# Optimization experiments

Measured on AMD Instinct MI355X. Metric: run time of the kernel, lower is better.

The kernel has to match this reference:

```python
import jax, jax.numpy as jnp
from jax import lax
import numpy as np


def setup_inputs() -> dict:
    key = jax.random.key(0)
    k1, k2, k3, k4 = jax.random.split(key, 4)
    X = jax.random.normal(k1, (2_000_000, 20), dtype=jnp.float32)
    W = jax.random.normal(k2, (20, 20), dtype=jnp.float32) * 0.1  # Linear weight
    b = jax.random.normal(k3, (20,), dtype=jnp.float32) * 0.1     # Linear bias
    rand_weight = jax.random.uniform(k4, (20, 20), dtype=jnp.float32)  # fixed, non-trainable
    return {"X": X, "W": W, "b": b, "rand_weight": rand_weight}


def reference(X, W, b, rand_weight):
    # X = self.liner(X)  -> torch Linear: X @ W.T + b
    h = X @ W.T + b
    # X = relu(X @ rand_weight + 1)
    h = jax.nn.relu(h @ rand_weight + 1.0)
    # (second self.liner(X) in the source is computed but unused -> omitted)
    # while X.abs().sum() > 1: X /= 2  -- count halvings, then apply once.
    s0 = jnp.sum(jnp.abs(h))
    def cond(c):
        _, s = c
        return s > 1.0
    def body(c):
        n, s = c
        return n + 1, s * 0.5
    n, _ = lax.while_loop(cond, body, (jnp.int32(0), s0))
    h = h * jnp.exp2(-n.astype(h.dtype))  # exact power-of-two scaling == repeated /2
    return jnp.sum(h)
```

## Files before the change

### kernel.cpp

```cpp
#include <hip/hip_runtime.h>


#define D 20
#define BLOCK 256
#define RPT 2
#define RPB (BLOCK * RPT)
#define F4PB (RPB * D / 4)
#define NLD (F4PB / BLOCK)
#define LDS_F4 (F4PB + F4PB / 10)
#define WS_PARTIALS_BYTES 32768


__global__ void setup_kernel(const float* __restrict__ W,
                             const float* __restrict__ b,
                             const float* __restrict__ RW,
                             float* __restrict__ Mt,
                             float* __restrict__ dvec,
                             unsigned* __restrict__ counter) {
    const int tid = threadIdx.x;
    if (tid == 0) *counter = 0u;
    for (int idx = tid; idx < D * D; idx += blockDim.x) {
        const int j = idx / D, k = idx % D;
        float s = 0.0f;
        for (int i = 0; i < D; ++i)
            s = fmaf(W[i * D + k], RW[i * D + j], s);
        Mt[idx] = s;
    }
    if (tid < D) {
        float s = 1.0f;
        for (int i = 0; i < D; ++i)
            s = fmaf(b[i], RW[i * D + tid], s);
        dvec[tid] = s;
    }
}

__global__ void __launch_bounds__(BLOCK)
fused_mlp_sum(const float* __restrict__ X,
              const float* __restrict__ Mt,
              const float* __restrict__ dvec,
              double* __restrict__ partials,
              unsigned* __restrict__ counter,
              float* __restrict__ out,
              int nrows) {
    __shared__ float4 lds4[LDS_F4];
    __shared__ float wave_sums[BLOCK / 64];
    __shared__ double dsum[BLOCK / 64];
    __shared__ int is_last;

    const int tid = threadIdx.x;
    const int bid = blockIdx.x;

    const long long total_f4 = ((long long)nrows * D) >> 2;
    const long long base_f4 = (long long)bid * F4PB;
    const long long rem = total_f4 - base_f4;
    const int chunk_f4 = (rem < (long long)F4PB) ? (int)rem : F4PB;
    const float4* __restrict__ xg = (const float4*)X + base_f4;

#pragma unroll
    for (int q = 0; q < NLD; ++q) {
        const int s = tid + BLOCK * q;
        const int sc = (s < chunk_f4) ? s : (chunk_f4 - 1);
        lds4[s + s / 10] = xg[sc];
    }
    __syncthreads();

    float x0[D], x1[D];
    const int b4 = 11 * tid;
#pragma unroll
    for (int q = 0; q < 5; ++q) {
        const float4 v = lds4[b4 + q];
        x0[4 * q + 0] = v.x; x0[4 * q + 1] = v.y;
        x0[4 * q + 2] = v.z; x0[4 * q + 3] = v.w;
        const float4 u = lds4[b4 + 5 + q];
        x1[4 * q + 0] = u.x; x1[4 * q + 1] = u.y;
        x1[4 * q + 2] = u.z; x1[4 * q + 3] = u.w;
    }

    float lsum = 0.0f;
#pragma unroll
    for (int j = 0; j < D; ++j) {
        float t0 = dvec[j];
        float t1 = t0;
#pragma unroll
        for (int k = 0; k < D; ++k) {
            const float m = Mt[j * D + k];
            t0 = fmaf(x0[k], m, t0);
            t1 = fmaf(x1[k], m, t1);
        }
        lsum += fmaxf(t0, 0.0f) + fmaxf(t1, 0.0f);
    }
    const bool valid = (long long)bid * RPB + 2 * tid < (long long)nrows;
    lsum = valid ? lsum : 0.0f;

#pragma unroll
    for (int off = 32; off > 0; off >>= 1)
        lsum += __shfl_down(lsum, off, 64);
    if ((tid & 63) == 0) wave_sums[tid >> 6] = lsum;
    __syncthreads();

    if (tid == 0) {
        float bs = wave_sums[0] + wave_sums[1] + wave_sums[2] + wave_sums[3];
        __hip_atomic_store(&partials[bid], (double)bs, __ATOMIC_RELEASE,
                           __HIP_MEMORY_SCOPE_AGENT);
        const unsigned t = __hip_atomic_fetch_add(counter, 1u, __ATOMIC_ACQ_REL,
                                                  __HIP_MEMORY_SCOPE_AGENT);
        is_last = (t == gridDim.x - 1);
    }
    __syncthreads();

    if (is_last) {
        double s = 0.0;
        for (int i = tid; i < (int)gridDim.x; i += BLOCK)
            s += __hip_atomic_load(&partials[i], __ATOMIC_RELAXED,
                                   __HIP_MEMORY_SCOPE_AGENT);
#pragma unroll
        for (int off = 32; off > 0; off >>= 1)
            s += __shfl_down(s, off, 64);
        if ((tid & 63) == 0) dsum[tid >> 6] = s;
        __syncthreads();
        if (tid == 0) {
            const double s0 = dsum[0] + dsum[1] + dsum[2] + dsum[3];
            float f = (float)s0;
            while (f > 1.0f) f *= 0.5f;
            out[0] = f;
        }
    }
}

extern "C" void kernel_launch(void* const* d_in, const int* in_sizes, int n_in,
                              void* d_out, int out_size, void* d_ws, size_t ws_size,
                              hipStream_t stream) {
    const float* X  = (const float*)d_in[0];
    const float* W  = (const float*)d_in[1];
    const float* b  = (const float*)d_in[2];
    const float* RW = (const float*)d_in[3];
    float* out = (float*)d_out;

    double* partials = (double*)d_ws;
    float*  Mt = (float*)((char*)d_ws + WS_PARTIALS_BYTES);
    float*  dv = Mt + D * D;
    unsigned* counter = (unsigned*)((char*)d_ws + WS_PARTIALS_BYTES + 1600 + 80);

    const int nrows = in_sizes[0] / (D * 4);

    setup_kernel<<<1, 256, 0, stream>>>(W, b, RW, Mt, dv, counter);

    const int blocks = (nrows + RPB - 1) / RPB;
    fused_mlp_sum<<<blocks, BLOCK, 0, stream>>>(X, Mt, dv, partials, counter,
                                                out, nrows);
}
```

Measured before the change: 227.1 us.

## Use persistent grid with direct global-to-LDS loads and per-wave chunk buffers

```diff
diff --git a/kernel.cpp b/kernel.cpp
--- a/kernel.cpp
+++ b/kernel.cpp
@@ -3,13 +3,20 @@
 
 #define D 20
 #define BLOCK 256
-#define RPT 2
-#define RPB (BLOCK * RPT)
-#define F4PB (RPB * D / 4)
-#define NLD (F4PB / BLOCK)
-#define LDS_F4 (F4PB + F4PB / 10)
+#define CHUNK_ROWS 256
+#define CHUNK_F4 (CHUNK_ROWS * D / 4)
+#define WAVE_F4 (CHUNK_F4 / 4)
+#define GRID 2048
 #define WS_PARTIALS_BYTES 32768
 
+#define GLOBAL_AS __attribute__((address_space(1)))
+#define LDS_AS    __attribute__((address_space(3)))
+
+
+__device__ __forceinline__ void gload16(const float4* g, float4* l) {
+    __builtin_amdgcn_global_load_lds((const GLOBAL_AS void*)g,
+                                     (LDS_AS void*)l, 16, 0, 0);
+}
 
 __global__ void setup_kernel(const float* __restrict__ W,
                              const float* __restrict__ b,
@@ -34,7 +41,7 @@
     }
 }
 
-__global__ void __launch_bounds__(BLOCK)
+__global__ void __launch_bounds__(BLOCK, 6)
 fused_mlp_sum(const float* __restrict__ X,
               const float* __restrict__ Mt,
               const float* __restrict__ dvec,
@@ -42,81 +49,78 @@
               unsigned* __restrict__ counter,
               float* __restrict__ out,
               int nrows) {
-    __shared__ float4 lds4[LDS_F4];
+    __shared__ float4 lds4[CHUNK_F4];
     __shared__ float wave_sums[BLOCK / 64];
     __shared__ double dsum[BLOCK / 64];
     __shared__ int is_last;
 
-    const int tid = threadIdx.x;
-    const int bid = blockIdx.x;
-
-    const long long total_f4 = ((long long)nrows * D) >> 2;
-    const long long base_f4 = (long long)bid * F4PB;
-    const long long rem = total_f4 - base_f4;
-    const int chunk_f4 = (rem < (long long)F4PB) ? (int)rem : F4PB;
-    const float4* __restrict__ xg = (const float4*)X + base_f4;
-
-#pragma unroll
-    for (int q = 0; q < NLD; ++q) {
-        const int s = tid + BLOCK * q;
-        const int sc = (s < chunk_f4) ? s : (chunk_f4 - 1);
-        lds4[s + s / 10] = xg[sc];
-    }
-    __syncthreads();
-
-    float x0[D], x1[D];
-    const int b4 = 11 * tid;
-#pragma unroll
-    for (int q = 0; q < 5; ++q) {
-        const float4 v = lds4[b4 + q];
-        x0[4 * q + 0] = v.x; x0[4 * q + 1] = v.y;
-        x0[4 * q + 2] = v.z; x0[4 * q + 3] = v.w;
-        const float4 u = lds4[b4 + 5 + q];
-        x1[4 * q + 0] = u.x; x1[4 * q + 1] = u.y;
-        x1[4 * q + 2] = u.z; x1[4 * q + 3] = u.w;
-    }
+    const int tid  = threadIdx.x;
+    const int lane = tid & 63;
+    const int wave = tid >> 6;
+    const int bid  = blockIdx.x;
+    const int G    = gridDim.x;
+    const long long max_f4 = (((long long)nrows * D) >> 2) - 1;
+    const int nchunks = (nrows + CHUNK_ROWS - 1) / CHUNK_ROWS;
+    const float4* __restrict__ xg4 = (const float4*)X;
+    float4* const wbuf = lds4 + wave * WAVE_F4;
 
     float lsum = 0.0f;
+    for (int c = bid; c < nchunks; c += G) {
+        const long long base = (long long)c * CHUNK_F4 + wave * WAVE_F4;
 #pragma unroll
-    for (int j = 0; j < D; ++j) {
-        float t0 = dvec[j];
-        float t1 = t0;
+        for (int i = 0; i < 5; ++i) {
+            long long s = base + i * 64 + lane;
+            s = (s <= max_f4) ? s : max_f4;
+            gload16(xg4 + s, wbuf + i * 64);
+        }
+        asm volatile("s_waitcnt vmcnt(0)" ::: "memory");
+        __builtin_amdgcn_sched_barrier(0);
+
+        const float4* row = wbuf + 5 * lane;
+        float x[D];
 #pragma unroll
-        for (int k = 0; k < D; ++k) {
-            const float m = Mt[j * D + k];
-            t0 = fmaf(x0[k], m, t0);
-            t1 = fmaf(x1[k], m, t1);
+        for (int q = 0; q < 5; ++q) {
+            const float4 v = row[q];
+            x[4 * q + 0] = v.x; x[4 * q + 1] = v.y;
+            x[4 * q + 2] = v.z; x[4 * q + 3] = v.w;
         }
-        lsum += fmaxf(t0, 0.0f) + fmaxf(t1, 0.0f);
+        float rs = 0.0f;
+#pragma unroll
+        for (int j = 0; j < D; ++j) {
+            float t = dvec[j];
+#pragma unroll
+            for (int k = 0; k < D; ++k)
+                t = fmaf(x[k], Mt[j * D + k], t);
+            rs += fmaxf(t, 0.0f);
+        }
+        lsum += ((long long)c * CHUNK_ROWS + tid < (long long)nrows) ? rs : 0.0f;
     }
-    const bool valid = (long long)bid * RPB + 2 * tid < (long long)nrows;
-    lsum = valid ? lsum : 0.0f;
 
 #pragma unroll
     for (int off = 32; off > 0; off >>= 1)
         lsum += __shfl_down(lsum, off, 64);
-    if ((tid & 63) == 0) wave_sums[tid >> 6] = lsum;
+    if (lane == 0) wave_sums[wave] = lsum;
     __syncthreads();
 
     if (tid == 0) {
-        float bs = wave_sums[0] + wave_sums[1] + wave_sums[2] + wave_sums[3];
+        const float bs = wave_sums[0] + wave_sums[1] + wave_sums[2] + wave_sums[3];
         __hip_atomic_store(&partials[bid], (double)bs, __ATOMIC_RELEASE,
                            __HIP_MEMORY_SCOPE_AGENT);
         const unsigned t = __hip_atomic_fetch_add(counter, 1u, __ATOMIC_ACQ_REL,
                                                   __HIP_MEMORY_SCOPE_AGENT);
-        is_last = (t == gridDim.x - 1);
+        is_last = (t == (unsigned)(G - 1));
     }
     __syncthreads();
 
     if (is_last) {
-        double s = 0.0;
-        for (int i = tid; i < (int)gridDim.x; i += BLOCK)
-            s += __hip_atomic_load(&partials[i], __ATOMIC_RELAXED,
-                                   __HIP_MEMORY_SCOPE_AGENT);
+        double sd = 0.0;
+        for (int i = tid; i < G; i += BLOCK)
+            sd += __hip_atomic_load(&partials[i], __ATOMIC_RELAXED,
+                                    __HIP_MEMORY_SCOPE_AGENT);
 #pragma unroll
         for (int off = 32; off > 0; off >>= 1)
-            s += __shfl_down(s, off, 64);
-        if ((tid & 63) == 0) dsum[tid >> 6] = s;
+            sd += __shfl_down(sd, off, 64);
+        if (lane == 0) dsum[wave] = sd;
         __syncthreads();
         if (tid == 0) {
             const double s0 = dsum[0] + dsum[1] + dsum[2] + dsum[3];
@@ -145,7 +149,6 @@
 
     setup_kernel<<<1, 256, 0, stream>>>(W, b, RW, Mt, dv, counter);
 
-    const int blocks = (nrows + RPB - 1) / RPB;
-    fused_mlp_sum<<<blocks, BLOCK, 0, stream>>>(X, Mt, dv, partials, counter,
-                                                out, nrows);
+    fused_mlp_sum<<<GRID, BLOCK, 0, stream>>>(X, Mt, dv, partials, counter,
+                                              out, nrows);
 }
```

Measured after the change: 265.3 us. 1.17x slower.
